# Optimization experiments

Hardware: AMD Instinct MI355X
Metric: run time of the kernel (lower is better)

The kernel has to match this reference:

```python
import jax, jax.numpy as jnp
import numpy as np

DIM = 1024
EPS_LN = 1e-5
EPS_MEM = 1e-6

def _layernorm(x, g, b):
    mu = jnp.mean(x, axis=-1, keepdims=True)
    var = jnp.mean((x - mu) ** 2, axis=-1, keepdims=True)
    return (x - mu) * jax.lax.rsqrt(var + EPS_LN) * g + b

def setup_inputs() -> dict:
    key = jax.random.key(0)
    ks = jax.random.split(key, 8)
    B, S, D = 4, 4096, DIM
    s1 = 1.0 / np.sqrt(D)
    s2 = 1.0 / np.sqrt(4 * D)
    return {
        "x": jax.random.normal(ks[0], (B, S, D), dtype=jnp.float32),
        "ln1_g": jnp.ones((D,), jnp.float32),
        "ln1_b": jnp.zeros((D,), jnp.float32),
        "ln2_g": jnp.ones((D,), jnp.float32),
        "ln2_b": jnp.zeros((D,), jnp.float32),
        "gate_w": jax.random.uniform(ks[1], (D, D), jnp.float32, -s1, s1),
        "gate_b": jax.random.uniform(ks[2], (D,), jnp.float32, -s1, s1),
        "value_w": jax.random.uniform(ks[3], (D, D), jnp.float32, -s1, s1),
        "value_b": jax.random.uniform(ks[4], (D,), jnp.float32, -s1, s1),
        "ffn_w1": jax.random.uniform(ks[5], (D, 4 * D), jnp.float32, -s1, s1),
        "ffn_b1": jnp.zeros((4 * D,), jnp.float32),
        "ffn_w2": jax.random.uniform(ks[6], (4 * D, D), jnp.float32, -s2, s2),
        "ffn_b2": jnp.zeros((D,), jnp.float32),
    }

def reference(x, ln1_g, ln1_b, ln2_g, ln2_b, gate_w, gate_b, value_w, value_b, ffn_w1, ffn_b1, ffn_w2, ffn_b2):
    h = _layernorm(x, ln1_g, ln1_b)
    g = jax.nn.sigmoid(h @ gate_w + gate_b)
    v = h @ value_w + value_b
    cumsum_v = jnp.cumsum(g * v, axis=1)
    cumsum_g = jnp.cumsum(g, axis=1) + EPS_MEM
    x = x + cumsum_v / cumsum_g
    h2 = _layernorm(x, ln2_g, ln2_b)
    ffn = jax.nn.gelu(h2 @ ffn_w1 + ffn_b1, approximate=False) @ ffn_w2 + ffn_b2
    return x + ffn
```

## Files before the change

kernel.cpp:

```cpp
#include <hip/hip_runtime.h>
#include <cstdint>
#include <cstddef>

#define D_MODEL 1024
#define SEQ     4096
#define BATCH   4
#define M_ROWS  (BATCH*SEQ)
#define NCHUNK  64
#define LCHUNK  (SEQ/NCHUNK)

typedef __bf16 bf16_t;
typedef __bf16 bf16x8 __attribute__((ext_vector_type(8)));
typedef __bf16 bf16x4 __attribute__((ext_vector_type(4)));
typedef float  f32x4  __attribute__((ext_vector_type(4)));

__device__ __forceinline__ void load_lds_128(const bf16_t* g, bf16_t* l) {
    __builtin_amdgcn_global_load_lds(
        (const __attribute__((address_space(1))) unsigned int*)g,
        (__attribute__((address_space(3))) unsigned int*)l,
        16, 0, 0);
}

__device__ __forceinline__ float2 bf16pair_to_f2(unsigned int u) {
    union { unsigned int i; float f; } a, b;
    a.i = u << 16;
    b.i = u & 0xffff0000u;
    float2 r; r.x = a.f; r.y = b.f; return r;
}

__global__ __launch_bounds__(256)
void transpose_all(const float* __restrict__ gate_w, const float* __restrict__ value_w,
                   const float* __restrict__ ffn_w1, const float* __restrict__ ffn_w2,
                   bf16_t* __restrict__ wgv_t, bf16_t* __restrict__ w1_t,
                   bf16_t* __restrict__ w2_t) {
    int id = blockIdx.x;
    const float* in; bf16_t* outp; int R, C, bx, by;
    if (id < 1024)      { in = gate_w;  outp = wgv_t;               R = 1024; C = 1024; bx = id & 31;  by = id >> 5; }
    else if (id < 2048) { id -= 1024; in = value_w; outp = wgv_t + 1024*1024; R = 1024; C = 1024; bx = id & 31;  by = id >> 5; }
    else if (id < 6144) { id -= 2048; in = ffn_w1;  outp = w1_t;    R = 1024; C = 4096; bx = id & 127; by = id >> 7; }
    else                { id -= 6144; in = ffn_w2;  outp = w2_t;    R = 4096; C = 1024; bx = id & 31;  by = id >> 5; }
    __shared__ float t[32][33];
    int tx = threadIdx.x & 31, ty = threadIdx.x >> 5;
    int c0 = bx * 32, r0 = by * 32;
    #pragma unroll
    for (int j = 0; j < 32; j += 8)
        t[ty + j][tx] = in[(size_t)(r0 + ty + j) * C + c0 + tx];
    __syncthreads();
    #pragma unroll
    for (int j = 0; j < 32; j += 8)
        outp[(size_t)(c0 + ty + j) * R + r0 + tx] = (bf16_t)t[tx][ty + j];
}

__global__ __launch_bounds__(256)
void ln_kernel(const float* __restrict__ x, const float* __restrict__ gamma,
               const float* __restrict__ beta, bf16_t* __restrict__ h) {
    int row = blockIdx.x;
    int tid = threadIdx.x;
    const float4* xr = (const float4*)(x + (size_t)row * D_MODEL);
    float4 v = xr[tid];
    float s  = v.x + v.y + v.z + v.w;
    float ss = v.x*v.x + v.y*v.y + v.z*v.z + v.w*v.w;
    #pragma unroll
    for (int off = 32; off; off >>= 1) {
        s  += __shfl_down(s, off);
        ss += __shfl_down(ss, off);
    }
    __shared__ float red[8];
    int wave = tid >> 6, lane = tid & 63;
    if (lane == 0) { red[wave] = s; red[4 + wave] = ss; }
    __syncthreads();
    if (tid == 0) {
        float S  = red[0] + red[1] + red[2] + red[3];
        float SS = red[4] + red[5] + red[6] + red[7];
        float mean = S * (1.0f / D_MODEL);
        float var  = SS * (1.0f / D_MODEL) - mean * mean;
        red[0] = mean;
        red[1] = rsqrtf(var + 1e-5f);
    }
    __syncthreads();
    float mean = red[0], rstd = red[1];
    float4 gv = ((const float4*)gamma)[tid];
    float4 bv = ((const float4*)beta)[tid];
    bf16x4 o;
    o[0] = (bf16_t)((v.x - mean) * rstd * gv.x + bv.x);
    o[1] = (bf16_t)((v.y - mean) * rstd * gv.y + bv.y);
    o[2] = (bf16_t)((v.z - mean) * rstd * gv.z + bv.z);
    o[3] = (bf16_t)((v.w - mean) * rstd * gv.w + bv.w);
    ((bf16x4*)h)[(size_t)row * (D_MODEL / 4) + tid] = o;
}

template <int MODE, int TN>
__global__ __launch_bounds__(256, 4)
void gemm_kernel(const bf16_t* __restrict__ A, const bf16_t* __restrict__ Bt,
                 const float* __restrict__ bias, const float* __restrict__ bias2,
                 const float* __restrict__ xres,
                 void* __restrict__ out, void* __restrict__ out2,
                 int M, int N, int K) {
    __shared__ __align__(16) bf16_t ldsA[128 * 64];
    __shared__ __align__(16) bf16_t ldsB[128 * 64];

    const int tid  = threadIdx.x;
    const int lane = tid & 63;
    const int wave = tid >> 6;
    const int wm   = wave & 1;
    const int wn   = wave >> 1;

    const int L  = blockIdx.x;
    const int r  = L >> 3;
    const int n0 = (r % TN) * 128;
    const int m0 = ((L & 7) + 8 * (r / TN)) * 128;

    f32x4 acc[4][4];
    f32x4 zero = {0.f, 0.f, 0.f, 0.f};
    #pragma unroll
    for (int i = 0; i < 4; i++)
        #pragma unroll
        for (int j = 0; j < 4; j++) acc[i][j] = zero;

    const int rl     = lane >> 3;
    const int srcCol = ((lane & 7) ^ rl) * 8;

    const int quad = lane >> 4;
    const int l16  = lane & 15;
    const int rswz = l16 & 7;

    for (int k0 = 0; k0 < K; k0 += 64) {
        __syncthreads();
        #pragma unroll
        for (int i = 0; i < 4; i++) {
            int cb = i * 4 + wave;
            int rr = cb * 8 + rl;
            load_lds_128(A  + (size_t)(m0 + rr) * K + k0 + srcCol,
                         ldsA + cb * 512 + lane * 8);
            load_lds_128(Bt + (size_t)(n0 + rr) * K + k0 + srcCol,
                         ldsB + cb * 512 + lane * 8);
        }
        __syncthreads();

        #pragma unroll
        for (int kk = 0; kk < 2; kk++) {
            int pos = ((quad + 4 * kk) ^ rswz) * 8;
            bf16x8 af[4], bfr[4];
            #pragma unroll
            for (int mt = 0; mt < 4; mt++)
                af[mt] = *(const bf16x8*)(ldsA + (wm * 64 + mt * 16 + l16) * 64 + pos);
            #pragma unroll
            for (int nt = 0; nt < 4; nt++)
                bfr[nt] = *(const bf16x8*)(ldsB + (wn * 64 + nt * 16 + l16) * 64 + pos);
            #pragma unroll
            for (int mt = 0; mt < 4; mt++)
                #pragma unroll
                for (int nt = 0; nt < 4; nt++)
                    acc[mt][nt] = __builtin_amdgcn_mfma_f32_16x16x32_bf16(
                        bfr[nt], af[mt], acc[mt][nt], 0, 0, 0);
        }
    }

    #pragma unroll
    for (int mt = 0; mt < 4; mt++) {
        int row = m0 + wm * 64 + mt * 16 + l16;
        #pragma unroll
        for (int nt = 0; nt < 4; nt++) {
            int col = n0 + wn * 64 + nt * 16 + quad * 4;
            f32x4 a = acc[mt][nt];
            if (MODE == 4) {
                bool isV = (n0 >= 1024);
                int c1 = col & 1023;
                float4 bv = *(const float4*)((isV ? bias2 : bias) + c1);
                float4 val;
                val.x = a[0] + bv.x; val.y = a[1] + bv.y;
                val.z = a[2] + bv.z; val.w = a[3] + bv.w;
                if (!isV) {
                    val.x = 1.0f / (1.0f + __expf(-val.x));
                    val.y = 1.0f / (1.0f + __expf(-val.y));
                    val.z = 1.0f / (1.0f + __expf(-val.z));
                    val.w = 1.0f / (1.0f + __expf(-val.w));
                }
                bf16x4 p;
                p[0] = (bf16_t)val.x; p[1] = (bf16_t)val.y;
                p[2] = (bf16_t)val.z; p[3] = (bf16_t)val.w;
                bf16_t* o = (bf16_t*)(isV ? out2 : out);
                *(bf16x4*)(o + (size_t)row * 1024 + c1) = p;
            } else if (MODE == 2) {
                float4 bv = *(const float4*)(bias + col);
                float4 val;
                val.x = a[0] + bv.x; val.y = a[1] + bv.y;
                val.z = a[2] + bv.z; val.w = a[3] + bv.w;
                val.x = 0.5f * val.x * (1.0f + erff(val.x * 0.70710678118654752f));
                val.y = 0.5f * val.y * (1.0f + erff(val.y * 0.70710678118654752f));
                val.z = 0.5f * val.z * (1.0f + erff(val.z * 0.70710678118654752f));
                val.w = 0.5f * val.w * (1.0f + erff(val.w * 0.70710678118654752f));
                bf16x4 p;
                p[0] = (bf16_t)val.x; p[1] = (bf16_t)val.y;
                p[2] = (bf16_t)val.z; p[3] = (bf16_t)val.w;
                *(bf16x4*)((bf16_t*)out + (size_t)row * N + col) = p;
            } else {
                float4 bv = *(const float4*)(bias + col);
                float4 xr = *(const float4*)(xres + (size_t)row * N + col);
                float4 val;
                val.x = xr.x + a[0] + bv.x; val.y = xr.y + a[1] + bv.y;
                val.z = xr.z + a[2] + bv.z; val.w = xr.w + a[3] + bv.w;
                *(float4*)((float*)out + (size_t)row * N + col) = val;
            }
        }
    }
}

__global__ __launch_bounds__(256)
void scan_partial(const bf16_t* __restrict__ g, const bf16_t* __restrict__ v,
                  float* __restrict__ sg, float* __restrict__ sgv) {
    int dt = blockIdx.x & 1;
    int c  = (blockIdx.x >> 1) & (NCHUNK - 1);
    int b  = blockIdx.x >> 7;
    int d  = dt * 512 + threadIdx.x * 2;
    float s0 = 0.f, s1 = 0.f, t0 = 0.f, t1 = 0.f;
    for (int i = 0; i < LCHUNK; i++) {
        int s = c * LCHUNK + i;
        size_t idx = ((size_t)(b * SEQ + s)) * D_MODEL + d;
        float2 gf = bf16pair_to_f2(*(const unsigned int*)(g + idx));
        float2 vf = bf16pair_to_f2(*(const unsigned int*)(v + idx));
        s0 += gf.x; s1 += gf.y;
        t0 += gf.x * vf.x; t1 += gf.y * vf.y;
    }
    size_t o = ((size_t)(b * NCHUNK + c)) * D_MODEL + d;
    sg[o] = s0;  sg[o + 1] = s1;
    sgv[o] = t0; sgv[o + 1] = t1;
}

__global__ __launch_bounds__(256)
void scan_apply(const bf16_t* __restrict__ g, const bf16_t* __restrict__ v,
                const float* __restrict__ x, const float* __restrict__ sg,
                const float* __restrict__ sgv, float* __restrict__ out) {
    int dt = blockIdx.x & 1;
    int c  = (blockIdx.x >> 1) & (NCHUNK - 1);
    int b  = blockIdx.x >> 7;
    int d  = dt * 512 + threadIdx.x * 2;
    float rg0 = 0.f, rg1 = 0.f, rv0 = 0.f, rv1 = 0.f;
    for (int p = 0; p < c; p++) {
        size_t o = ((size_t)(b * NCHUNK + p)) * D_MODEL + d;
        float2 a  = *(const float2*)(sg + o);
        float2 bb = *(const float2*)(sgv + o);
        rg0 += a.x;  rg1 += a.y;
        rv0 += bb.x; rv1 += bb.y;
    }
    for (int i = 0; i < LCHUNK; i++) {
        int s = c * LCHUNK + i;
        size_t idx = ((size_t)(b * SEQ + s)) * D_MODEL + d;
        float2 gf = bf16pair_to_f2(*(const unsigned int*)(g + idx));
        float2 vf = bf16pair_to_f2(*(const unsigned int*)(v + idx));
        rv0 += gf.x * vf.x; rg0 += gf.x;
        rv1 += gf.y * vf.y; rg1 += gf.y;
        float2 xv = *(const float2*)(x + idx);
        float2 ov;
        ov.x = xv.x + rv0 / (rg0 + 1e-6f);
        ov.y = xv.y + rv1 / (rg1 + 1e-6f);
        *(float2*)(out + idx) = ov;
    }
}

extern "C" void kernel_launch(void* const* d_in, const int* in_sizes, int n_in,
                              void* d_out, int out_size, void* d_ws, size_t ws_size,
                              hipStream_t stream) {
    (void)in_sizes; (void)n_in; (void)out_size; (void)ws_size;
    const float* x       = (const float*)d_in[0];
    const float* ln1_g   = (const float*)d_in[1];
    const float* ln1_b   = (const float*)d_in[2];
    const float* ln2_g   = (const float*)d_in[3];
    const float* ln2_b   = (const float*)d_in[4];
    const float* gate_w  = (const float*)d_in[5];
    const float* gate_b  = (const float*)d_in[6];
    const float* value_w = (const float*)d_in[7];
    const float* value_b = (const float*)d_in[8];
    const float* ffn_w1  = (const float*)d_in[9];
    const float* ffn_b1  = (const float*)d_in[10];
    const float* ffn_w2  = (const float*)d_in[11];
    const float* ffn_b2  = (const float*)d_in[12];
    float* out = (float*)d_out;

    char* ws = (char*)d_ws;
    const size_t MB = 1024 * 1024;
    bf16_t* wgv_t = (bf16_t*)(ws + 0 * MB);
    bf16_t* w1_t  = (bf16_t*)(ws + 4 * MB);
    bf16_t* w2_t  = (bf16_t*)(ws + 12 * MB);
    bf16_t* h     = (bf16_t*)(ws + 20 * MB);
    bf16_t* g     = (bf16_t*)(ws + 52 * MB);
    bf16_t* v     = (bf16_t*)(ws + 84 * MB);
    float*  sg    = (float*)(ws + 116 * MB);
    float*  sgv   = (float*)(ws + 117 * MB);
    bf16_t* act   = (bf16_t*)(ws + 118 * MB);

    transpose_all<<<10240, 256, 0, stream>>>(gate_w, value_w, ffn_w1, ffn_w2,
                                             wgv_t, w1_t, w2_t);

    ln_kernel<<<M_ROWS, 256, 0, stream>>>(x, ln1_g, ln1_b, h);

    gemm_kernel<4, 16><<<(2048 / 128) * (M_ROWS / 128), 256, 0, stream>>>(
        h, wgv_t, gate_b, value_b, nullptr, g, v, M_ROWS, 2048, 1024);

    scan_partial<<<BATCH * NCHUNK * 2, 256, 0, stream>>>(g, v, sg, sgv);
    scan_apply<<<BATCH * NCHUNK * 2, 256, 0, stream>>>(g, v, x, sg, sgv, out);

    ln_kernel<<<M_ROWS, 256, 0, stream>>>(out, ln2_g, ln2_b, h);

    gemm_kernel<2, 32><<<(4096 / 128) * (M_ROWS / 128), 256, 0, stream>>>(
        h, w1_t, ffn_b1, nullptr, nullptr, act, nullptr, M_ROWS, 4096, 1024);

    gemm_kernel<3, 8><<<(1024 / 128) * (M_ROWS / 128), 256, 0, stream>>>(
        act, w2_t, ffn_b2, nullptr, out, out, nullptr, M_ROWS, 1024, 4096);
}
```

Baseline: 631.7 us.

## Fuse weight prep with LN1, scan-apply with LN2, and use tanh-form GELU

The weight transpose and the first layernorm now run as one launch, with a block-index split deciding which job each block does. The scan-apply step now also computes the second layernorm row by row, so the residual output is not re-read by a separate LN kernel. Each block handles a full 1024-wide row chunk and does a block reduction with a double-buffered shared array per row. The exact erf GELU in the FFN1 epilogue is replaced by the tanh approximation written in sigmoid form, which slightly changes numerics. The fused scan launches half as many blocks and adds a barrier for every row, which may reduce parallelism.

```diff
diff --git a/kernel.cpp b/kernel.cpp
--- a/kernel.cpp
+++ b/kernel.cpp
@@ -28,65 +28,70 @@
     float2 r; r.x = a.f; r.y = b.f; return r;
 }
 
+__device__ __forceinline__ float fast_gelu(float x) {
+    float u = 1.5957691216057308f * (x + 0.044715f * x * x * x);
+    return x / (1.0f + __expf(-u));
+}
+
 __global__ __launch_bounds__(256)
-void transpose_all(const float* __restrict__ gate_w, const float* __restrict__ value_w,
-                   const float* __restrict__ ffn_w1, const float* __restrict__ ffn_w2,
-                   bf16_t* __restrict__ wgv_t, bf16_t* __restrict__ w1_t,
-                   bf16_t* __restrict__ w2_t) {
+void prep_kernel(const float* __restrict__ gate_w, const float* __restrict__ value_w,
+                 const float* __restrict__ ffn_w1, const float* __restrict__ ffn_w2,
+                 bf16_t* __restrict__ wgv_t, bf16_t* __restrict__ w1_t,
+                 bf16_t* __restrict__ w2_t,
+                 const float* __restrict__ x, const float* __restrict__ ln1_g,
+                 const float* __restrict__ ln1_b, bf16_t* __restrict__ h) {
     int id = blockIdx.x;
-    const float* in; bf16_t* outp; int R, C, bx, by;
-    if (id < 1024)      { in = gate_w;  outp = wgv_t;               R = 1024; C = 1024; bx = id & 31;  by = id >> 5; }
-    else if (id < 2048) { id -= 1024; in = value_w; outp = wgv_t + 1024*1024; R = 1024; C = 1024; bx = id & 31;  by = id >> 5; }
-    else if (id < 6144) { id -= 2048; in = ffn_w1;  outp = w1_t;    R = 1024; C = 4096; bx = id & 127; by = id >> 7; }
-    else                { id -= 6144; in = ffn_w2;  outp = w2_t;    R = 4096; C = 1024; bx = id & 31;  by = id >> 5; }
-    __shared__ float t[32][33];
-    int tx = threadIdx.x & 31, ty = threadIdx.x >> 5;
-    int c0 = bx * 32, r0 = by * 32;
-    #pragma unroll
-    for (int j = 0; j < 32; j += 8)
-        t[ty + j][tx] = in[(size_t)(r0 + ty + j) * C + c0 + tx];
-    __syncthreads();
-    #pragma unroll
-    for (int j = 0; j < 32; j += 8)
-        outp[(size_t)(c0 + ty + j) * R + r0 + tx] = (bf16_t)t[tx][ty + j];
-}
-
-__global__ __launch_bounds__(256)
-void ln_kernel(const float* __restrict__ x, const float* __restrict__ gamma,
-               const float* __restrict__ beta, bf16_t* __restrict__ h) {
-    int row = blockIdx.x;
     int tid = threadIdx.x;
-    const float4* xr = (const float4*)(x + (size_t)row * D_MODEL);
-    float4 v = xr[tid];
-    float s  = v.x + v.y + v.z + v.w;
-    float ss = v.x*v.x + v.y*v.y + v.z*v.z + v.w*v.w;
-    #pragma unroll
-    for (int off = 32; off; off >>= 1) {
-        s  += __shfl_down(s, off);
-        ss += __shfl_down(ss, off);
-    }
-    __shared__ float red[8];
-    int wave = tid >> 6, lane = tid & 63;
-    if (lane == 0) { red[wave] = s; red[4 + wave] = ss; }
-    __syncthreads();
-    if (tid == 0) {
-        float S  = red[0] + red[1] + red[2] + red[3];
-        float SS = red[4] + red[5] + red[6] + red[7];
-        float mean = S * (1.0f / D_MODEL);
-        float var  = SS * (1.0f / D_MODEL) - mean * mean;
-        red[0] = mean;
-        red[1] = rsqrtf(var + 1e-5f);
-    }
-    __syncthreads();
-    float mean = red[0], rstd = red[1];
-    float4 gv = ((const float4*)gamma)[tid];
-    float4 bv = ((const float4*)beta)[tid];
-    bf16x4 o;
-    o[0] = (bf16_t)((v.x - mean) * rstd * gv.x + bv.x);
-    o[1] = (bf16_t)((v.y - mean) * rstd * gv.y + bv.y);
-    o[2] = (bf16_t)((v.z - mean) * rstd * gv.z + bv.z);
-    o[3] = (bf16_t)((v.w - mean) * rstd * gv.w + bv.w);
-    ((bf16x4*)h)[(size_t)row * (D_MODEL / 4) + tid] = o;
+    if (id < 10240) {
+        const float* in; bf16_t* outp; int R, C, bx, by;
+        if (id < 1024)      { in = gate_w;  outp = wgv_t;               R = 1024; C = 1024; bx = id & 31;  by = id >> 5; }
+        else if (id < 2048) { id -= 1024; in = value_w; outp = wgv_t + 1024*1024; R = 1024; C = 1024; bx = id & 31;  by = id >> 5; }
+        else if (id < 6144) { id -= 2048; in = ffn_w1;  outp = w1_t;    R = 1024; C = 4096; bx = id & 127; by = id >> 7; }
+        else                { id -= 6144; in = ffn_w2;  outp = w2_t;    R = 4096; C = 1024; bx = id & 31;  by = id >> 5; }
+        __shared__ float t[32][33];
+        int tx = tid & 31, ty = tid >> 5;
+        int c0 = bx * 32, r0 = by * 32;
+        #pragma unroll
+        for (int j = 0; j < 32; j += 8)
+            t[ty + j][tx] = in[(size_t)(r0 + ty + j) * C + c0 + tx];
+        __syncthreads();
+        #pragma unroll
+        for (int j = 0; j < 32; j += 8)
+            outp[(size_t)(c0 + ty + j) * R + r0 + tx] = (bf16_t)t[tx][ty + j];
+    } else {
+        int row = id - 10240;
+        const float4* xr = (const float4*)(x + (size_t)row * D_MODEL);
+        float4 v = xr[tid];
+        float s  = v.x + v.y + v.z + v.w;
+        float ss = v.x*v.x + v.y*v.y + v.z*v.z + v.w*v.w;
+        #pragma unroll
+        for (int off = 32; off; off >>= 1) {
+            s  += __shfl_down(s, off);
+            ss += __shfl_down(ss, off);
+        }
+        __shared__ float red[8];
+        int wave = tid >> 6, lane = tid & 63;
+        if (lane == 0) { red[wave] = s; red[4 + wave] = ss; }
+        __syncthreads();
+        if (tid == 0) {
+            float S  = red[0] + red[1] + red[2] + red[3];
+            float SS = red[4] + red[5] + red[6] + red[7];
+            float mean = S * (1.0f / D_MODEL);
+            float var  = SS * (1.0f / D_MODEL) - mean * mean;
+            red[0] = mean;
+            red[1] = rsqrtf(var + 1e-5f);
+        }
+        __syncthreads();
+        float mean = red[0], rstd = red[1];
+        float4 gv = ((const float4*)ln1_g)[tid];
+        float4 bv = ((const float4*)ln1_b)[tid];
+        bf16x4 o;
+        o[0] = (bf16_t)((v.x - mean) * rstd * gv.x + bv.x);
+        o[1] = (bf16_t)((v.y - mean) * rstd * gv.y + bv.y);
+        o[2] = (bf16_t)((v.z - mean) * rstd * gv.z + bv.z);
+        o[3] = (bf16_t)((v.w - mean) * rstd * gv.w + bv.w);
+        ((bf16x4*)h)[(size_t)row * (D_MODEL / 4) + tid] = o;
+    }
 }
 
 template <int MODE, int TN>
@@ -183,16 +188,11 @@
                 *(bf16x4*)(o + (size_t)row * 1024 + c1) = p;
             } else if (MODE == 2) {
                 float4 bv = *(const float4*)(bias + col);
-                float4 val;
-                val.x = a[0] + bv.x; val.y = a[1] + bv.y;
-                val.z = a[2] + bv.z; val.w = a[3] + bv.w;
-                val.x = 0.5f * val.x * (1.0f + erff(val.x * 0.70710678118654752f));
-                val.y = 0.5f * val.y * (1.0f + erff(val.y * 0.70710678118654752f));
-                val.z = 0.5f * val.z * (1.0f + erff(val.z * 0.70710678118654752f));
-                val.w = 0.5f * val.w * (1.0f + erff(val.w * 0.70710678118654752f));
                 bf16x4 p;
-                p[0] = (bf16_t)val.x; p[1] = (bf16_t)val.y;
-                p[2] = (bf16_t)val.z; p[3] = (bf16_t)val.w;
+                p[0] = (bf16_t)fast_gelu(a[0] + bv.x);
+                p[1] = (bf16_t)fast_gelu(a[1] + bv.y);
+                p[2] = (bf16_t)fast_gelu(a[2] + bv.z);
+                p[3] = (bf16_t)fast_gelu(a[3] + bv.w);
                 *(bf16x4*)((bf16_t*)out + (size_t)row * N + col) = p;
             } else {
                 float4 bv = *(const float4*)(bias + col);
@@ -228,33 +228,67 @@
 }
 
 __global__ __launch_bounds__(256)
-void scan_apply(const bf16_t* __restrict__ g, const bf16_t* __restrict__ v,
-                const float* __restrict__ x, const float* __restrict__ sg,
-                const float* __restrict__ sgv, float* __restrict__ out) {
-    int dt = blockIdx.x & 1;
-    int c  = (blockIdx.x >> 1) & (NCHUNK - 1);
-    int b  = blockIdx.x >> 7;
-    int d  = dt * 512 + threadIdx.x * 2;
-    float rg0 = 0.f, rg1 = 0.f, rv0 = 0.f, rv1 = 0.f;
+void scan_ln2(const bf16_t* __restrict__ g, const bf16_t* __restrict__ v,
+              const float* __restrict__ x, const float* __restrict__ sg,
+              const float* __restrict__ sgv,
+              const float* __restrict__ ln2_g, const float* __restrict__ ln2_b,
+              float* __restrict__ out, bf16_t* __restrict__ h2) {
+    int c  = blockIdx.x & (NCHUNK - 1);
+    int b  = blockIdx.x >> 6;
+    int tid = threadIdx.x;
+    int d  = tid * 4;
+    int wv = tid >> 6, lane = tid & 63;
+
+    f32x4 rg = {0.f, 0.f, 0.f, 0.f}, rv = {0.f, 0.f, 0.f, 0.f};
     for (int p = 0; p < c; p++) {
         size_t o = ((size_t)(b * NCHUNK + p)) * D_MODEL + d;
-        float2 a  = *(const float2*)(sg + o);
-        float2 bb = *(const float2*)(sgv + o);
-        rg0 += a.x;  rg1 += a.y;
-        rv0 += bb.x; rv1 += bb.y;
-    }
+        rg += *(const f32x4*)(sg + o);
+        rv += *(const f32x4*)(sgv + o);
+    }
+
+    float4 gam = ((const float4*)ln2_g)[tid];
+    float4 bet = ((const float4*)ln2_b)[tid];
+
+    __shared__ float red[2][8];
     for (int i = 0; i < LCHUNK; i++) {
-        int s = c * LCHUNK + i;
-        size_t idx = ((size_t)(b * SEQ + s)) * D_MODEL + d;
-        float2 gf = bf16pair_to_f2(*(const unsigned int*)(g + idx));
-        float2 vf = bf16pair_to_f2(*(const unsigned int*)(v + idx));
-        rv0 += gf.x * vf.x; rg0 += gf.x;
-        rv1 += gf.y * vf.y; rg1 += gf.y;
-        float2 xv = *(const float2*)(x + idx);
-        float2 ov;
-        ov.x = xv.x + rv0 / (rg0 + 1e-6f);
-        ov.y = xv.y + rv1 / (rg1 + 1e-6f);
-        *(float2*)(out + idx) = ov;
+        size_t idx = ((size_t)(b * SEQ + c * LCHUNK + i)) * D_MODEL + d;
+        uint2 gu = *(const uint2*)(g + idx);
+        uint2 vu = *(const uint2*)(v + idx);
+        float2 g01 = bf16pair_to_f2(gu.x), g23 = bf16pair_to_f2(gu.y);
+        float2 v01 = bf16pair_to_f2(vu.x), v23 = bf16pair_to_f2(vu.y);
+        rg[0] += g01.x; rv[0] += g01.x * v01.x;
+        rg[1] += g01.y; rv[1] += g01.y * v01.y;
+        rg[2] += g23.x; rv[2] += g23.x * v23.x;
+        rg[3] += g23.y; rv[3] += g23.y * v23.y;
+        f32x4 xv = *(const f32x4*)(x + idx);
+        f32x4 xn;
+        xn[0] = xv[0] + rv[0] / (rg[0] + 1e-6f);
+        xn[1] = xv[1] + rv[1] / (rg[1] + 1e-6f);
+        xn[2] = xv[2] + rv[2] / (rg[2] + 1e-6f);
+        xn[3] = xv[3] + rv[3] / (rg[3] + 1e-6f);
+        *(f32x4*)(out + idx) = xn;
+
+        float s  = xn[0] + xn[1] + xn[2] + xn[3];
+        float ss = xn[0]*xn[0] + xn[1]*xn[1] + xn[2]*xn[2] + xn[3]*xn[3];
+        #pragma unroll
+        for (int off = 32; off; off >>= 1) {
+            s  += __shfl_down(s, off);
+            ss += __shfl_down(ss, off);
+        }
+        int buf = i & 1;
+        if (lane == 0) { red[buf][wv] = s; red[buf][4 + wv] = ss; }
+        __syncthreads();
+        float S  = red[buf][0] + red[buf][1] + red[buf][2] + red[buf][3];
+        float SS = red[buf][4] + red[buf][5] + red[buf][6] + red[buf][7];
+        float mean = S * (1.0f / D_MODEL);
+        float var  = SS * (1.0f / D_MODEL) - mean * mean;
+        float rstd = rsqrtf(var + 1e-5f);
+        bf16x4 o;
+        o[0] = (bf16_t)((xn[0] - mean) * rstd * gam.x + bet.x);
+        o[1] = (bf16_t)((xn[1] - mean) * rstd * gam.y + bet.y);
+        o[2] = (bf16_t)((xn[2] - mean) * rstd * gam.z + bet.z);
+        o[3] = (bf16_t)((xn[3] - mean) * rstd * gam.w + bet.w);
+        *(bf16x4*)(h2 + idx) = o;
     }
 }
 
@@ -289,18 +323,17 @@
     float*  sgv   = (float*)(ws + 117 * MB);
     bf16_t* act   = (bf16_t*)(ws + 118 * MB);
 
-    transpose_all<<<10240, 256, 0, stream>>>(gate_w, value_w, ffn_w1, ffn_w2,
-                                             wgv_t, w1_t, w2_t);
-
-    ln_kernel<<<M_ROWS, 256, 0, stream>>>(x, ln1_g, ln1_b, h);
+    prep_kernel<<<10240 + M_ROWS, 256, 0, stream>>>(
+        gate_w, value_w, ffn_w1, ffn_w2, wgv_t, w1_t, w2_t,
+        x, ln1_g, ln1_b, h);
 
     gemm_kernel<4, 16><<<(2048 / 128) * (M_ROWS / 128), 256, 0, stream>>>(
         h, wgv_t, gate_b, value_b, nullptr, g, v, M_ROWS, 2048, 1024);
 
     scan_partial<<<BATCH * NCHUNK * 2, 256, 0, stream>>>(g, v, sg, sgv);
-    scan_apply<<<BATCH * NCHUNK * 2, 256, 0, stream>>>(g, v, x, sg, sgv, out);
-
-    ln_kernel<<<M_ROWS, 256, 0, stream>>>(out, ln2_g, ln2_b, h);
+
+    scan_ln2<<<BATCH * NCHUNK, 256, 0, stream>>>(g, v, x, sg, sgv,
+                                                 ln2_g, ln2_b, out, h);
 
     gemm_kernel<2, 32><<<(4096 / 128) * (M_ROWS / 128), 256, 0, stream>>>(
         h, w1_t, ffn_b1, nullptr, nullptr, act, nullptr, M_ROWS, 4096, 1024);
```

Measured after the change: 643.2 us. About the same (+1.8%).
